# Performance work log

Hardware: AMD Instinct MI355X
Metric: run time of the kernel (lower is better)

Reference implementation:

```python
import jax, jax.numpy as jnp
import numpy as np

N_NODES = 100000


def gcn_conv(x, src, dst, W, b, n_nodes):
    """PyG GCNConv: add self-loops, symmetric deg^-1/2 normalization,
    linear transform, scatter-add aggregation, bias."""
    loop = jnp.arange(n_nodes, dtype=src.dtype)
    s = jnp.concatenate([src, loop])
    d = jnp.concatenate([dst, loop])
    # degree of destination nodes (includes self-loops)
    deg = jax.ops.segment_sum(jnp.ones(s.shape[0], dtype=x.dtype), d,
                              num_segments=n_nodes)
    dis = jnp.where(deg > 0, jax.lax.rsqrt(deg), 0.0)  # deg^-1/2
    norm = dis[s] * dis[d]                              # [E+N]
    h = x @ W                                           # [N, out]
    msg = h[s] * norm[:, None]                          # gather + scale
    out = jax.ops.segment_sum(msg, d, num_segments=n_nodes)  # scatter-add
    return out + b


def setup_inputs() -> dict:
    key = jax.random.key(0)
    k1, k2, k3, k4 = jax.random.split(key, 4)
    F_in, H, C = 500, 64, 10
    x = jax.random.normal(k1, (N_NODES, F_in), dtype=jnp.float32)
    edge_index = jax.random.randint(k2, (2, 1600000), 0, N_NODES,
                                    dtype=jnp.int32)
    W1 = jax.random.normal(k3, (F_in, H), dtype=jnp.float32) / np.sqrt(F_in)
    b1 = jnp.zeros((H,), dtype=jnp.float32)
    W2 = jax.random.normal(k4, (H, C), dtype=jnp.float32) / np.sqrt(H)
    b2 = jnp.zeros((C,), dtype=jnp.float32)
    return {"x": x, "edge_index": edge_index,
            "W1": W1, "b1": b1, "W2": W2, "b2": b2}


def reference(x, edge_index, W1, b1, W2, b2):
    src, dst = edge_index[0], edge_index[1]
    h = gcn_conv(x, src, dst, W1, b1, N_NODES)
    h = jax.nn.relu(h)
    # dropout is identity at inference (training=False)
    out = gcn_conv(h, src, dst, W2, b2, N_NODES)
    return out
```

## Files before the change

kernel.cpp:

```cpp
#include <hip/hip_runtime.h>

#define F_IN 500
#define HDIM 64
#define CDIM 10
#define KPAD 512
#define NSTAGE 16
#define H2LD 16

typedef __attribute__((ext_vector_type(8))) short bf16x8;
typedef __attribute__((ext_vector_type(4))) float floatx4;

__device__ inline unsigned short f2bf(float f) {
    unsigned int u = __float_as_uint(f);
    u += 0x7fffu + ((u >> 16) & 1u);
    return (unsigned short)(u >> 16);
}
__device__ inline float bflo(unsigned int u) { return __uint_as_float(u << 16); }
__device__ inline float bfhi(unsigned int u) { return __uint_as_float(u & 0xffff0000u); }

__global__ __launch_bounds__(256) void prep_kernel(
        const int* __restrict__ dst, int E, int* __restrict__ deg,
        const float* __restrict__ W1, unsigned short* __restrict__ whf,
        unsigned short* __restrict__ wlf, int degB) {
    int bid = blockIdx.x;
    if (bid < degB) {
        int e = bid * 256 + threadIdx.x;
        if (e < E) atomicAdd(&deg[dst[e]], 1);
    } else {
        int idx = (bid - degB) * 256 + threadIdx.x;
        if (idx >= KPAD * HDIM) return;
        int k = idx >> 6;
        int f = idx & 63;
        float w = (k < F_IN) ? W1[k * HDIM + f] : 0.f;
        unsigned int b = __float_as_uint(w);
        unsigned short hh = (unsigned short)(b >> 16);
        float wl = w - __uint_as_float(b & 0xffff0000u);
        unsigned short ll = (unsigned short)(__float_as_uint(wl) >> 16);
        int kb = k >> 5, q = (k >> 3) & 3, j = k & 7;
        int fb = f >> 4, fl = f & 15;
        int lane = (q << 4) | fl;
        size_t o = ((((size_t)kb * 4 + fb) * 64 + lane) << 3) | (size_t)j;
        whf[o] = hh;
        wlf[o] = ll;
    }
}

__global__ void scan_block_kernel(const int* __restrict__ deg,
                                  int* __restrict__ row_ptr,
                                  int* __restrict__ blk_sum,
                                  float* __restrict__ dis, int Np1) {
    __shared__ int wsum[16];
    int i = blockIdx.x * 1024 + threadIdx.x;
    int v = (i < Np1 - 1) ? deg[i] : 0;
    if (i < Np1 - 1) dis[i] = rsqrtf((float)(v + 1));
    int lane = threadIdx.x & 63;
    int wid = threadIdx.x >> 6;
    int x = v;
#pragma unroll
    for (int off = 1; off < 64; off <<= 1) {
        int y = __shfl_up(x, off);
        if (lane >= off) x += y;
    }
    if (lane == 63) wsum[wid] = x;
    __syncthreads();
    if (threadIdx.x < 16) {
        int ws = wsum[threadIdx.x];
#pragma unroll
        for (int off = 1; off < 16; off <<= 1) {
            int y = __shfl_up(ws, off);
            if ((int)threadIdx.x >= off) ws += y;
        }
        wsum[threadIdx.x] = ws;
    }
    __syncthreads();
    int wp = (wid > 0) ? wsum[wid - 1] : 0;
    if (i < Np1) row_ptr[i] = wp + x - v;
    if (threadIdx.x == 1023) blk_sum[blockIdx.x] = wp + x;
}

__global__ void scan_top_kernel(int* __restrict__ blk_sum, int nb) {
    int carry = 0;
    for (int base = 0; base < nb; base += 64) {
        int i = base + (int)threadIdx.x;
        int v = (i < nb) ? blk_sum[i] : 0;
        int x = v;
#pragma unroll
        for (int off = 1; off < 64; off <<= 1) {
            int y = __shfl_up(x, off);
            if ((int)threadIdx.x >= off) x += y;
        }
        if (i < nb) blk_sum[i] = carry + x - v;
        carry += __shfl(x, 63);
    }
}

__global__ __launch_bounds__(256) void csr_gemm_kernel(
        const float* __restrict__ x, const unsigned short* __restrict__ whf,
        const unsigned short* __restrict__ wlf, const float* __restrict__ dis,
        unsigned short* __restrict__ h1b, int N,
        const int* __restrict__ src, const int* __restrict__ dst,
        const int* __restrict__ row_ptr, const int* __restrict__ blk_sum,
        int* __restrict__ cursor, int* __restrict__ csr_src, int E,
        int gemmB) {
    const int bid = blockIdx.x;
    if (bid >= gemmB) {
        int e = (bid - gemmB) * 256 + threadIdx.x;
        if (e >= E) return;
        int d = dst[e];
        int pos = atomicAdd(&cursor[d], 1);
        csr_src[row_ptr[d] + blk_sum[d >> 10] + pos] = src[e];
        return;
    }
    const int lane = threadIdx.x & 63;
    const int wid = (bid * 256 + threadIdx.x) >> 6;
    const int n0 = wid * 32;
    if (n0 >= N) return;
    const int q = lane >> 4;
    const int fl = lane & 15;

    int r0 = n0 + fl;       if (r0 >= N) r0 = N - 1;
    int r1 = n0 + 16 + fl;  if (r1 >= N) r1 = N - 1;
    const float* xp0 = x + (size_t)r0 * F_IN + q * 8;
    const float* xp1 = x + (size_t)r1 * F_IN + q * 8;

    floatx4 acc[2][4];
#pragma unroll
    for (int t = 0; t < 2; ++t)
#pragma unroll
        for (int fb = 0; fb < 4; ++fb) acc[t][fb] = (floatx4){0.f, 0.f, 0.f, 0.f};

    const bf16x8* whv = (const bf16x8*)whf;
    const bf16x8* wlv = (const bf16x8*)wlf;

    for (int kb = 0; kb < NSTAGE; ++kb) {
        float xv0[8], xv1[8];
        if (kb < NSTAGE - 1) {
            float4 a = *(const float4*)(xp0 + kb * 32);
            float4 b = *(const float4*)(xp0 + kb * 32 + 4);
            xv0[0] = a.x; xv0[1] = a.y; xv0[2] = a.z; xv0[3] = a.w;
            xv0[4] = b.x; xv0[5] = b.y; xv0[6] = b.z; xv0[7] = b.w;
            float4 c = *(const float4*)(xp1 + kb * 32);
            float4 d = *(const float4*)(xp1 + kb * 32 + 4);
            xv1[0] = c.x; xv1[1] = c.y; xv1[2] = c.z; xv1[3] = c.w;
            xv1[4] = d.x; xv1[5] = d.y; xv1[6] = d.z; xv1[7] = d.w;
        } else {
#pragma unroll
            for (int j = 0; j < 8; ++j) {
                int kk = kb * 32 + q * 8 + j;
                xv0[j] = (kk < F_IN) ? xp0[kb * 32 + j] : 0.f;
                xv1[j] = (kk < F_IN) ? xp1[kb * 32 + j] : 0.f;
            }
        }
        bf16x8 xh0, xl0, xh1, xl1;
#pragma unroll
        for (int j = 0; j < 8; ++j) {
            unsigned int b0 = __float_as_uint(xv0[j]);
            xh0[j] = (short)(b0 >> 16);
            float res0 = xv0[j] - __uint_as_float(b0 & 0xffff0000u);
            xl0[j] = (short)(__float_as_uint(res0) >> 16);
            unsigned int b1 = __float_as_uint(xv1[j]);
            xh1[j] = (short)(b1 >> 16);
            float res1 = xv1[j] - __uint_as_float(b1 & 0xffff0000u);
            xl1[j] = (short)(__float_as_uint(res1) >> 16);
        }
#pragma unroll
        for (int fb = 0; fb < 4; ++fb) {
            bf16x8 bh = whv[(size_t)(kb * 4 + fb) * 64 + lane];
            bf16x8 bl = wlv[(size_t)(kb * 4 + fb) * 64 + lane];
            acc[0][fb] = __builtin_amdgcn_mfma_f32_16x16x32_bf16(xh0, bh, acc[0][fb], 0, 0, 0);
            acc[0][fb] = __builtin_amdgcn_mfma_f32_16x16x32_bf16(xl0, bh, acc[0][fb], 0, 0, 0);
            acc[0][fb] = __builtin_amdgcn_mfma_f32_16x16x32_bf16(xh0, bl, acc[0][fb], 0, 0, 0);
            acc[1][fb] = __builtin_amdgcn_mfma_f32_16x16x32_bf16(xh1, bh, acc[1][fb], 0, 0, 0);
            acc[1][fb] = __builtin_amdgcn_mfma_f32_16x16x32_bf16(xl1, bh, acc[1][fb], 0, 0, 0);
            acc[1][fb] = __builtin_amdgcn_mfma_f32_16x16x32_bf16(xh1, bl, acc[1][fb], 0, 0, 0);
        }
    }
#pragma unroll
    for (int t = 0; t < 2; ++t) {
#pragma unroll
        for (int r = 0; r < 4; ++r) {
            int node = n0 + t * 16 + q * 4 + r;
            if (node < N) {
                float dn = dis[node];
#pragma unroll
                for (int fb = 0; fb < 4; ++fb) {
                    h1b[(size_t)node * HDIM + fb * 16 + fl] =
                        f2bf(acc[t][fb][r] * dn);
                }
            }
        }
    }
}

__global__ __launch_bounds__(256) void gather1_kernel(
        const int* __restrict__ row_ptr, const int* __restrict__ blk_sum,
        const int* __restrict__ csr_src, const float* __restrict__ dis,
        const unsigned short* __restrict__ h1b,
        float* __restrict__ agg1, int N) {
    int nid = blockIdx.x * 4 + (threadIdx.x >> 6);
    if (nid >= N) return;
    int node = __builtin_amdgcn_readfirstlane(nid);
    int lane = threadIdx.x & 63;
    int half = lane >> 5;
    int c = lane & 31;
    int beg = row_ptr[node] + blk_sum[node >> 10];
    int end = row_ptr[node + 1] + blk_sum[(node + 1) >> 10];
    float dd = dis[node];
    float a0 = 0.f, a1 = 0.f;
    if (half == 0) {
        unsigned int w = *reinterpret_cast<const unsigned int*>(
            h1b + (size_t)node * HDIM + 2 * c);
        a0 = bflo(w);
        a1 = bfhi(w);
    }
    int p = beg + half;
    for (; p + 14 < end; p += 16) {
        unsigned int wv[8];
#pragma unroll
        for (int i = 0; i < 8; ++i) {
            int s = csr_src[p + 2 * i];
            wv[i] = *reinterpret_cast<const unsigned int*>(
                h1b + (size_t)s * HDIM + 2 * c);
        }
#pragma unroll
        for (int i = 0; i < 8; ++i) {
            a0 += bflo(wv[i]);
            a1 += bfhi(wv[i]);
        }
    }
    for (; p < end; p += 2) {
        int s0 = csr_src[p];
        unsigned int w0 = *reinterpret_cast<const unsigned int*>(
            h1b + (size_t)s0 * HDIM + 2 * c);
        a0 += bflo(w0);
        a1 += bfhi(w0);
    }
    a0 += __shfl_xor(a0, 32);
    a1 += __shfl_xor(a1, 32);
    if (half == 0) {
        *reinterpret_cast<float2*>(agg1 + (size_t)node * HDIM + 2 * c) =
            make_float2(a0 * dd, a1 * dd);
    }
}

__global__ void layer2_kernel(const float* __restrict__ agg1,
                              const float* __restrict__ b1,
                              const float* __restrict__ W2,
                              const float* __restrict__ dis,
                              float* __restrict__ h2s, int N) {
    int n = blockIdx.x * blockDim.x + threadIdx.x;
    if (n >= N) return;
    const float* ar = agg1 + (size_t)n * HDIM;
    float t[HDIM];
#pragma unroll
    for (int c = 0; c < HDIM; ++c) {
        float v = ar[c] + b1[c];
        t[c] = v > 0.f ? v : 0.f;
    }
    float dn = dis[n];
    float* h2r = h2s + (size_t)n * H2LD;
#pragma unroll
    for (int j = 0; j < CDIM; ++j) {
        float acc = 0.f;
#pragma unroll
        for (int c = 0; c < HDIM; ++c) acc = fmaf(t[c], W2[c * CDIM + j], acc);
        h2r[j] = acc * dn;
    }
}

__global__ __launch_bounds__(256) void gather2_kernel(
        const int* __restrict__ row_ptr, const int* __restrict__ blk_sum,
        const int* __restrict__ csr_src, const float* __restrict__ dis,
        const float* __restrict__ h2s, const float* __restrict__ b2,
        float* __restrict__ out, int N) {
    int nid = blockIdx.x * 4 + (threadIdx.x >> 6);
    if (nid >= N) return;
    int node = __builtin_amdgcn_readfirstlane(nid);
    int lane = threadIdx.x & 63;
    int g = lane >> 4;
    int j = lane & 15;
    int beg = row_ptr[node] + blk_sum[node >> 10];
    int end = row_ptr[node + 1] + blk_sum[(node + 1) >> 10];
    float acc = 0.f;
    int p = beg + g;
    for (; p + 12 < end; p += 16) {
        int s0 = csr_src[p];
        int s1 = csr_src[p + 4];
        int s2 = csr_src[p + 8];
        int s3 = csr_src[p + 12];
        float v0 = (j < CDIM) ? h2s[(size_t)s0 * H2LD + j] : 0.f;
        float v1 = (j < CDIM) ? h2s[(size_t)s1 * H2LD + j] : 0.f;
        float v2 = (j < CDIM) ? h2s[(size_t)s2 * H2LD + j] : 0.f;
        float v3 = (j < CDIM) ? h2s[(size_t)s3 * H2LD + j] : 0.f;
        acc += (v0 + v1) + (v2 + v3);
    }
    for (; p < end; p += 4) {
        int s0 = csr_src[p];
        acc += (j < CDIM) ? h2s[(size_t)s0 * H2LD + j] : 0.f;
    }
    acc += __shfl_xor(acc, 16);
    acc += __shfl_xor(acc, 32);
    if (lane < CDIM) {
        float dd = dis[node];
        out[(size_t)node * CDIM + lane] =
            b2[lane] + dd * (acc + h2s[(size_t)node * H2LD + lane]);
    }
}

static inline char* align256(char* p) {
    return (char*)(((uintptr_t)p + 255) & ~(uintptr_t)255);
}

extern "C" void kernel_launch(void* const* d_in, const int* in_sizes, int n_in,
                              void* d_out, int out_size, void* d_ws,
                              size_t ws_size, hipStream_t stream) {
    const float* x  = (const float*)d_in[0];
    const int*   ei = (const int*)d_in[1];
    const float* W1 = (const float*)d_in[2];
    const float* b1 = (const float*)d_in[3];
    const float* W2 = (const float*)d_in[4];
    const float* b2 = (const float*)d_in[5];

    const int N = in_sizes[0] / F_IN;
    const int E = in_sizes[1] / 2;
    const int* src = ei;
    const int* dst = ei + E;
    float* out = (float*)d_out;

    const int Np1 = N + 1;
    const int nscan_blocks = (Np1 + 1023) / 1024;

    char* w = (char*)d_ws;
    int* deg = (int*)w;                  w = align256(w + (size_t)N * 4);
    int* cursor = (int*)w;               w = align256(w + (size_t)N * 4);
    char* zero_end = w;
    float* dis = (float*)w;              w = align256(w + (size_t)N * 4);
    int* row_ptr = (int*)w;              w = align256(w + (size_t)(N + 4) * 4);
    int* blk_sum = (int*)w;              w = align256(w + (size_t)nscan_blocks * 4);
    int* csr_src = (int*)w;              w = align256(w + (size_t)E * 4);
    unsigned short* whf = (unsigned short*)w;  w = align256(w + (size_t)KPAD * HDIM * 2);
    unsigned short* wlf = (unsigned short*)w;  w = align256(w + (size_t)KPAD * HDIM * 2);
    unsigned short* h1b = (unsigned short*)w;  w = align256(w + (size_t)N * HDIM * 2);
    float* agg1 = (float*)w;             w = align256(w + (size_t)N * HDIM * 4);
    float* h2s = (float*)w;              w = align256(w + (size_t)N * H2LD * 4);

    hipMemsetAsync(deg, 0, (size_t)(zero_end - (char*)deg), stream);

    const int degB = (E + 255) / 256;
    const int wprepB = (KPAD * HDIM + 255) / 256;
    prep_kernel<<<degB + wprepB, 256, 0, stream>>>(dst, E, deg, W1, whf, wlf,
                                                   degB);
    scan_block_kernel<<<nscan_blocks, 1024, 0, stream>>>(deg, row_ptr, blk_sum,
                                                         dis, Np1);
    scan_top_kernel<<<1, 64, 0, stream>>>(blk_sum, nscan_blocks);
    {
        int gemmB = ((N + 31) / 32 + 3) / 4;
        int csrB = (E + 255) / 256;
        csr_gemm_kernel<<<gemmB + csrB, 256, 0, stream>>>(
            x, whf, wlf, dis, h1b, N,
            src, dst, row_ptr, blk_sum, cursor, csr_src, E, gemmB);
    }
    gather1_kernel<<<(N + 3) / 4, 256, 0, stream>>>(row_ptr, blk_sum, csr_src,
                                                    dis, h1b, agg1, N);
    layer2_kernel<<<(N + 255) / 256, 256, 0, stream>>>(agg1, b1, W2, dis, h2s,
                                                       N);
    gather2_kernel<<<(N + 3) / 4, 256, 0, stream>>>(row_ptr, blk_sum, csr_src,
                                                    dis, h2s, b2, out, N);
}
```

Baseline: 563.2 us.

## Reuse degree-atomic ranks for CSR fill, interleave GEMM blocks, prefetch x

The degree-counting atomic now records each edge's rank within its destination row. The CSR fill pass uses that rank instead of issuing a second atomicAdd on a cursor array, and the cursor buffer is dropped. GEMM and CSR-fill blocks in the fused kernel are interleaved one in nine so both kinds of work run together across the GPU instead of GEMM blocks being scheduled first. The GEMM loop also software-prefetches the next x tile into registers. The cost is an extra E-sized rank array written and read, plus more register pressure from the prefetch.

```diff
diff --git a/kernel.cpp b/kernel.cpp
--- a/kernel.cpp
+++ b/kernel.cpp
@@ -20,12 +20,13 @@
 
 __global__ __launch_bounds__(256) void prep_kernel(
         const int* __restrict__ dst, int E, int* __restrict__ deg,
+        int* __restrict__ erank,
         const float* __restrict__ W1, unsigned short* __restrict__ whf,
         unsigned short* __restrict__ wlf, int degB) {
     int bid = blockIdx.x;
     if (bid < degB) {
         int e = bid * 256 + threadIdx.x;
-        if (e < E) atomicAdd(&deg[dst[e]], 1);
+        if (e < E) erank[e] = atomicAdd(&deg[dst[e]], 1);
     } else {
         int idx = (bid - degB) * 256 + threadIdx.x;
         if (idx >= KPAD * HDIM) return;
@@ -99,20 +100,25 @@
         const unsigned short* __restrict__ wlf, const float* __restrict__ dis,
         unsigned short* __restrict__ h1b, int N,
         const int* __restrict__ src, const int* __restrict__ dst,
+        const int* __restrict__ erank,
         const int* __restrict__ row_ptr, const int* __restrict__ blk_sum,
-        int* __restrict__ cursor, int* __restrict__ csr_src, int E,
+        int* __restrict__ csr_src, int E,
         int gemmB) {
     const int bid = blockIdx.x;
-    if (bid >= gemmB) {
-        int e = (bid - gemmB) * 256 + threadIdx.x;
+    const int g9 = bid / 9;
+    const bool isGemm = (bid % 9 == 0) && (g9 < gemmB);
+    if (!isGemm) {
+        int before = (bid + 8) / 9;
+        if (before > gemmB) before = gemmB;
+        int cb = bid - before;
+        int e = cb * 256 + threadIdx.x;
         if (e >= E) return;
         int d = dst[e];
-        int pos = atomicAdd(&cursor[d], 1);
-        csr_src[row_ptr[d] + blk_sum[d >> 10] + pos] = src[e];
+        csr_src[row_ptr[d] + blk_sum[d >> 10] + erank[e]] = src[e];
         return;
     }
     const int lane = threadIdx.x & 63;
-    const int wid = (bid * 256 + threadIdx.x) >> 6;
+    const int wid = (g9 * 256 + threadIdx.x) >> 6;
     const int n0 = wid * 32;
     if (n0 >= N) return;
     const int q = lane >> 4;
@@ -132,24 +138,53 @@
     const bf16x8* whv = (const bf16x8*)whf;
     const bf16x8* wlv = (const bf16x8*)wlf;
 
-    for (int kb = 0; kb < NSTAGE; ++kb) {
+    float4 na = *(const float4*)(xp0);
+    float4 nb = *(const float4*)(xp0 + 4);
+    float4 nc = *(const float4*)(xp1);
+    float4 nd = *(const float4*)(xp1 + 4);
+
+    for (int kb = 0; kb < NSTAGE - 1; ++kb) {
+        float4 a = na, b = nb, c = nc, d = nd;
+        if (kb + 1 < NSTAGE - 1) {
+            na = *(const float4*)(xp0 + (kb + 1) * 32);
+            nb = *(const float4*)(xp0 + (kb + 1) * 32 + 4);
+            nc = *(const float4*)(xp1 + (kb + 1) * 32);
+            nd = *(const float4*)(xp1 + (kb + 1) * 32 + 4);
+        }
+        float xv0[8] = {a.x, a.y, a.z, a.w, b.x, b.y, b.z, b.w};
+        float xv1[8] = {c.x, c.y, c.z, c.w, d.x, d.y, d.z, d.w};
+        bf16x8 xh0, xl0, xh1, xl1;
+#pragma unroll
+        for (int j = 0; j < 8; ++j) {
+            unsigned int b0 = __float_as_uint(xv0[j]);
+            xh0[j] = (short)(b0 >> 16);
+            float res0 = xv0[j] - __uint_as_float(b0 & 0xffff0000u);
+            xl0[j] = (short)(__float_as_uint(res0) >> 16);
+            unsigned int b1 = __float_as_uint(xv1[j]);
+            xh1[j] = (short)(b1 >> 16);
+            float res1 = xv1[j] - __uint_as_float(b1 & 0xffff0000u);
+            xl1[j] = (short)(__float_as_uint(res1) >> 16);
+        }
+#pragma unroll
+        for (int fb = 0; fb < 4; ++fb) {
+            bf16x8 bh = whv[(size_t)(kb * 4 + fb) * 64 + lane];
+            bf16x8 bl = wlv[(size_t)(kb * 4 + fb) * 64 + lane];
+            acc[0][fb] = __builtin_amdgcn_mfma_f32_16x16x32_bf16(xh0, bh, acc[0][fb], 0, 0, 0);
+            acc[0][fb] = __builtin_amdgcn_mfma_f32_16x16x32_bf16(xl0, bh, acc[0][fb], 0, 0, 0);
+            acc[0][fb] = __builtin_amdgcn_mfma_f32_16x16x32_bf16(xh0, bl, acc[0][fb], 0, 0, 0);
+            acc[1][fb] = __builtin_amdgcn_mfma_f32_16x16x32_bf16(xh1, bh, acc[1][fb], 0, 0, 0);
+            acc[1][fb] = __builtin_amdgcn_mfma_f32_16x16x32_bf16(xl1, bh, acc[1][fb], 0, 0, 0);
+            acc[1][fb] = __builtin_amdgcn_mfma_f32_16x16x32_bf16(xh1, bl, acc[1][fb], 0, 0, 0);
+        }
+    }
+    {
+        const int kb = NSTAGE - 1;
         float xv0[8], xv1[8];
-        if (kb < NSTAGE - 1) {
-            float4 a = *(const float4*)(xp0 + kb * 32);
-            float4 b = *(const float4*)(xp0 + kb * 32 + 4);
-            xv0[0] = a.x; xv0[1] = a.y; xv0[2] = a.z; xv0[3] = a.w;
-            xv0[4] = b.x; xv0[5] = b.y; xv0[6] = b.z; xv0[7] = b.w;
-            float4 c = *(const float4*)(xp1 + kb * 32);
-            float4 d = *(const float4*)(xp1 + kb * 32 + 4);
-            xv1[0] = c.x; xv1[1] = c.y; xv1[2] = c.z; xv1[3] = c.w;
-            xv1[4] = d.x; xv1[5] = d.y; xv1[6] = d.z; xv1[7] = d.w;
-        } else {
-#pragma unroll
-            for (int j = 0; j < 8; ++j) {
-                int kk = kb * 32 + q * 8 + j;
-                xv0[j] = (kk < F_IN) ? xp0[kb * 32 + j] : 0.f;
-                xv1[j] = (kk < F_IN) ? xp1[kb * 32 + j] : 0.f;
-            }
+#pragma unroll
+        for (int j = 0; j < 8; ++j) {
+            int kk = kb * 32 + q * 8 + j;
+            xv0[j] = (kk < F_IN) ? xp0[kb * 32 + j] : 0.f;
+            xv1[j] = (kk < F_IN) ? xp1[kb * 32 + j] : 0.f;
         }
         bf16x8 xh0, xl0, xh1, xl1;
 #pragma unroll
@@ -332,8 +367,8 @@
 
     char* w = (char*)d_ws;
     int* deg = (int*)w;                  w = align256(w + (size_t)N * 4);
-    int* cursor = (int*)w;               w = align256(w + (size_t)N * 4);
     char* zero_end = w;
+    int* erank = (int*)w;                w = align256(w + (size_t)E * 4);
     float* dis = (float*)w;              w = align256(w + (size_t)N * 4);
     int* row_ptr = (int*)w;              w = align256(w + (size_t)(N + 4) * 4);
     int* blk_sum = (int*)w;              w = align256(w + (size_t)nscan_blocks * 4);
@@ -348,8 +383,8 @@
 
     const int degB = (E + 255) / 256;
     const int wprepB = (KPAD * HDIM + 255) / 256;
-    prep_kernel<<<degB + wprepB, 256, 0, stream>>>(dst, E, deg, W1, whf, wlf,
-                                                   degB);
+    prep_kernel<<<degB + wprepB, 256, 0, stream>>>(dst, E, deg, erank, W1, whf,
+                                                   wlf, degB);
     scan_block_kernel<<<nscan_blocks, 1024, 0, stream>>>(deg, row_ptr, blk_sum,
                                                          dis, Np1);
     scan_top_kernel<<<1, 64, 0, stream>>>(blk_sum, nscan_blocks);
@@ -358,7 +393,7 @@
         int csrB = (E + 255) / 256;
         csr_gemm_kernel<<<gemmB + csrB, 256, 0, stream>>>(
             x, whf, wlf, dis, h1b, N,
-            src, dst, row_ptr, blk_sum, cursor, csr_src, E, gemmB);
+            src, dst, erank, row_ptr, blk_sum, csr_src, E, gemmB);
     }
     gather1_kernel<<<(N + 3) / 4, 256, 0, stream>>>(row_ptr, blk_sum, csr_src,
                                                     dis, h1b, agg1, N);
```

Result: faster. 543.2 us (-3.6%).
